# Optimization experiments

Hardware: AMD Instinct MI355X
Metric: run time of the kernel (lower is better)

Reference implementation:

```python
import jax, jax.numpy as jnp
import numpy as np

B, K, IN_DIM, H, D = 8, 4096, 512, 8, 64  # batch, tokens, in_dim, heads, per-head dim


def setup_inputs() -> dict:
    key = jax.random.key(0)
    ks = jax.random.split(key, 8)
    s = 0.02
    return {
        "x": jax.random.normal(ks[0], (B, K, IN_DIM), jnp.float32),
        "y": jax.random.normal(ks[1], (B, K, IN_DIM), jnp.float32),
        "Wq": jax.random.normal(ks[2], (IN_DIM, H * D), jnp.float32) * s,
        "bq": jnp.zeros((H * D,), jnp.float32),
        "Wk": jax.random.normal(ks[3], (IN_DIM, H * D), jnp.float32) * s,
        "bk": jnp.zeros((H * D,), jnp.float32),
        "Wv": jax.random.normal(ks[4], (IN_DIM, H * D), jnp.float32) * s,
        "bv": jnp.zeros((H * D,), jnp.float32),
        "Wp": jax.random.normal(ks[5], (IN_DIM, D), jnp.float32) * s,
        "gamma": jax.random.uniform(ks[6], (H, 1, 1, 1), jnp.float32) + 0.001,
    }


def _heads(t):
    # (B, K, H*D) -> (H, B, K, D); matches split_cat(t, D, dim=2, cat dim=0) head-major layout
    b, k, _ = t.shape
    return t.reshape(b, k, H, D).transpose(2, 0, 1, 3)


def reference(x, y, Wq, bq, Wk, bk, Wv, bv, Wp, gamma):
    q = _heads(x @ Wq + bq)   # (H,B,K,D)
    kk = _heads(x @ Wk + bk)  # (H,B,K,D)
    v = _heads(y @ Wv + bv)   # (H,B,K,D)
    # energy = q^T k contracted over tokens -> (H,B,D,D)
    energy = jnp.einsum('hbkd,hbke->hbde', q, kk)
    attn = jax.nn.softmax(energy, axis=-1)
    # out = v @ attn^T : out[k,q] = sum_e v[k,e] * attn[q,e]
    out = jnp.einsum('hbke,hbqe->hbkq', v, attn)  # (H,B,K,D)
    yp = y @ Wp  # projection(y): (B,K,D)
    out = (gamma * out + yp[None]) / (1.0 + gamma)
    return out.transpose(1, 0, 2, 3)  # (B,H,K,D)
```

## Files before the change

kernel.cpp:

```cpp
#include <hip/hip_runtime.h>

#define B_ 8
#define K_ 4096
#define IN_ 512
#define H_ 8
#define D_ 64
#define HD_ 512

typedef short bf16x8 __attribute__((ext_vector_type(8)));
typedef float f32x4 __attribute__((ext_vector_type(4)));
typedef unsigned short u16;
typedef unsigned short us8v __attribute__((ext_vector_type(8)));
typedef unsigned short us4v __attribute__((ext_vector_type(4)));

__device__ inline u16 f2bf_rn(float f) {
  unsigned u = __float_as_uint(f);
  u += 0x7fffu + ((u >> 16) & 1u);
  return (u16)(u >> 16);
}
__device__ inline float bf2f(u16 h) {
  return __uint_as_float(((unsigned)h) << 16);
}


__global__ __launch_bounds__(256) void k_cvt_x(const float* __restrict__ x,
                                               u16* __restrict__ xt_hi,
                                               u16* __restrict__ xt_lo,
                                               float* __restrict__ svec) {
  const int kt = blockIdx.x, ct = blockIdx.y, b = blockIdx.z;
  __shared__ float Xs[64][65];
  const int tid = threadIdx.x;
  const float* src = x + ((size_t)b * K_ + kt * 64) * IN_ + ct * 64;
#pragma unroll
  for (int r = 0; r < 4; ++r) {
    int idx = tid + 256 * r;
    int k = idx >> 4, c4 = (idx & 15) * 4;
    f32x4 v = *(const f32x4*)(src + (size_t)k * IN_ + c4);
    Xs[k][c4 + 0] = v[0];
    Xs[k][c4 + 1] = v[1];
    Xs[k][c4 + 2] = v[2];
    Xs[k][c4 + 3] = v[3];
  }
  __syncthreads();
  if (tid < 64) {
    float s = 0.f;
#pragma unroll
    for (int k = 0; k < 64; ++k) s += Xs[k][tid];
    atomicAdd(&svec[b * IN_ + ct * 64 + tid], s);
  }
#pragma unroll
  for (int r = 0; r < 2; ++r) {
    int idx = tid + 256 * r;
    int c = idx >> 3, ck = (idx & 7) * 8;
    us8v hv, lv;
#pragma unroll
    for (int j = 0; j < 8; ++j) {
      float f = Xs[ck + j][c];
      u16 h = f2bf_rn(f);
      float lo = f - bf2f(h);
      hv[j] = h;
      lv[j] = f2bf_rn(lo);
    }
    size_t off = ((size_t)(b * IN_ + ct * 64 + c)) * K_ + kt * 64 + ck;
    *(us8v*)(xt_hi + off) = hv;
    *(us8v*)(xt_lo + off) = lv;
  }
}

__global__ __launch_bounds__(256) void k_cvt_y(const float* __restrict__ y,
                                               u16* __restrict__ yb) {
  size_t i = ((size_t)blockIdx.x * 256 + threadIdx.x) * 8;
  f32x4 v0 = *(const f32x4*)(y + i);
  f32x4 v1 = *(const f32x4*)(y + i + 4);
  us8v o;
  o[0] = f2bf_rn(v0[0]); o[1] = f2bf_rn(v0[1]);
  o[2] = f2bf_rn(v0[2]); o[3] = f2bf_rn(v0[3]);
  o[4] = f2bf_rn(v1[0]); o[5] = f2bf_rn(v1[1]);
  o[6] = f2bf_rn(v1[2]); o[7] = f2bf_rn(v1[3]);
  *(us8v*)(yb + i) = o;
}

__global__ __launch_bounds__(256) void k_cvt_w(
    const float* __restrict__ Wq, const float* __restrict__ Wk,
    u16* __restrict__ Wqt_hi, u16* __restrict__ Wqt_lo,
    u16* __restrict__ Wkt_hi, u16* __restrict__ Wkt_lo) {
  const int ti = blockIdx.x, tj = blockIdx.y;
  const float* src = blockIdx.z ? Wk : Wq;
  u16* dhi = blockIdx.z ? Wkt_hi : Wqt_hi;
  u16* dlo = blockIdx.z ? Wkt_lo : Wqt_lo;
  __shared__ float T[64][65];
  const int tid = threadIdx.x;
#pragma unroll
  for (int r = 0; r < 4; ++r) {
    int idx = tid + 256 * r;
    int rr = idx >> 4, c4 = (idx & 15) * 4;
    f32x4 v = *(const f32x4*)(src + (size_t)(tj * 64 + rr) * 512 + ti * 64 + c4);
    T[rr][c4 + 0] = v[0]; T[rr][c4 + 1] = v[1];
    T[rr][c4 + 2] = v[2]; T[rr][c4 + 3] = v[3];
  }
  __syncthreads();
#pragma unroll
  for (int r = 0; r < 2; ++r) {
    int idx = tid + 256 * r;
    int d = idx >> 3, ck = (idx & 7) * 8;
    us8v hv, lv;
#pragma unroll
    for (int j = 0; j < 8; ++j) {
      float f = T[ck + j][d];
      u16 h = f2bf_rn(f);
      hv[j] = h;
      lv[j] = f2bf_rn(f - bf2f(h));
    }
    size_t off = (size_t)(ti * 64 + d) * 512 + tj * 64 + ck;
    *(us8v*)(dhi + off) = hv;
    *(us8v*)(dlo + off) = lv;
  }
}

#define GP 72

__global__ __launch_bounds__(256, 2) void k_gram_mfma(
    const u16* __restrict__ xt_hi, const u16* __restrict__ xt_lo,
    float* __restrict__ G) {
  int pp = blockIdx.x, ti = 0;
  while (pp >= 4 - ti) { pp -= 4 - ti; ++ti; }
  const int tj = ti + pp;
  const int b = blockIdx.y >> 3, kc = blockIdx.y & 7;
  __shared__ u16 Pih[128 * GP], Pil[128 * GP], Pjh[128 * GP], Pjl[128 * GP];
  const int tid = threadIdx.x;
  const int wave = tid >> 6, lane = tid & 63;
  const int wm = wave & 1, wn = wave >> 1;
  const int m16 = lane & 15, quad = lane >> 4;
  const size_t base_i = ((size_t)(b * IN_ + ti * 128)) * K_;
  const size_t base_j = ((size_t)(b * IN_ + tj * 128)) * K_;
  f32x4 zf = {0.f, 0.f, 0.f, 0.f};
  f32x4 acc[4][4];
#pragma unroll
  for (int mt = 0; mt < 4; ++mt)
#pragma unroll
    for (int nt = 0; nt < 4; ++nt) acc[mt][nt] = zf;
  const int kbeg = kc * 512, kend = kbeg + 512;

  us8v sih[4], sil[4], sjh[4], sjl[4];
  auto GLOAD = [&](int k0) {
#pragma unroll
    for (int r = 0; r < 4; ++r) {
      int idx = tid + 256 * r;
      int row = idx >> 3, ck = (idx & 7) * 8;
      size_t gi = base_i + (size_t)row * K_ + k0 + ck;
      size_t gj = base_j + (size_t)row * K_ + k0 + ck;
      sih[r] = *(const us8v*)(xt_hi + gi);
      sil[r] = *(const us8v*)(xt_lo + gi);
      sjh[r] = *(const us8v*)(xt_hi + gj);
      sjl[r] = *(const us8v*)(xt_lo + gj);
    }
  };
  auto SWRITE = [&]() {
#pragma unroll
    for (int r = 0; r < 4; ++r) {
      int idx = tid + 256 * r;
      int row = idx >> 3, ck = (idx & 7) * 8;
      int lo = row * GP + ck;
      *(us8v*)&Pih[lo] = sih[r];
      *(us8v*)&Pil[lo] = sil[r];
      *(us8v*)&Pjh[lo] = sjh[r];
      *(us8v*)&Pjl[lo] = sjl[r];
    }
  };

  GLOAD(kbeg);
  SWRITE();
  __syncthreads();
  for (int k0 = kbeg; k0 < kend; k0 += 64) {
    const bool more = (k0 + 64 < kend);
    if (more) GLOAD(k0 + 64);
#pragma unroll
    for (int kk = 0; kk < 64; kk += 32) {
      bf16x8 ah[4], al[4], bh[4], bl[4];
#pragma unroll
      for (int t = 0; t < 4; ++t) {
        int ar = (wm * 64 + t * 16 + m16) * GP + kk + quad * 8;
        ah[t] = *(const bf16x8*)&Pih[ar];
        al[t] = *(const bf16x8*)&Pil[ar];
        int br = (wn * 64 + t * 16 + m16) * GP + kk + quad * 8;
        bh[t] = *(const bf16x8*)&Pjh[br];
        bl[t] = *(const bf16x8*)&Pjl[br];
      }
#pragma unroll
      for (int mt = 0; mt < 4; ++mt)
#pragma unroll
        for (int nt = 0; nt < 4; ++nt) {
          acc[mt][nt] = __builtin_amdgcn_mfma_f32_16x16x32_bf16(
              ah[mt], bh[nt], acc[mt][nt], 0, 0, 0);
          acc[mt][nt] = __builtin_amdgcn_mfma_f32_16x16x32_bf16(
              ah[mt], bl[nt], acc[mt][nt], 0, 0, 0);
          acc[mt][nt] = __builtin_amdgcn_mfma_f32_16x16x32_bf16(
              al[mt], bh[nt], acc[mt][nt], 0, 0, 0);
        }
    }
    if (more) {
      __syncthreads();
      SWRITE();
      __syncthreads();
    }
  }
  float* Gb = G + (size_t)b * IN_ * IN_;
#pragma unroll
  for (int mt = 0; mt < 4; ++mt)
#pragma unroll
    for (int nt = 0; nt < 4; ++nt)
#pragma unroll
      for (int r = 0; r < 4; ++r) {
        int gi = ti * 128 + wm * 64 + mt * 16 + quad * 4 + r;
        int gj = tj * 128 + wn * 64 + nt * 16 + m16;
        atomicAdd(&Gb[(size_t)gi * IN_ + gj], acc[mt][nt][r]);
      }
}

__global__ __launch_bounds__(256) void k_cvt_g(const float* __restrict__ G,
                                               u16* __restrict__ Ghi,
                                               u16* __restrict__ Glo) {
  const int ti = blockIdx.x, tj = blockIdx.y, b = blockIdx.z;
  if (tj < ti) return;
  const float* Gb = G + (size_t)b * IN_ * IN_;
  u16* ghb = Ghi + (size_t)b * IN_ * IN_;
  u16* glb = Glo + (size_t)b * IN_ * IN_;
  __shared__ float T[64][65];
  const int tid = threadIdx.x;
#pragma unroll
  for (int r = 0; r < 4; ++r) {
    int idx = tid + 256 * r;
    int rr = idx >> 4, c4 = (idx & 15) * 4;
    f32x4 v = *(const f32x4*)(Gb + (size_t)(ti * 64 + rr) * IN_ + tj * 64 + c4);
    T[rr][c4 + 0] = v[0]; T[rr][c4 + 1] = v[1];
    T[rr][c4 + 2] = v[2]; T[rr][c4 + 3] = v[3];
  }
  __syncthreads();
#pragma unroll
  for (int r = 0; r < 2; ++r) {
    int idx = tid + 256 * r;
    int rr = idx >> 3, ck = (idx & 7) * 8;
    us8v hv, lv;
#pragma unroll
    for (int j = 0; j < 8; ++j) {
      float f = T[rr][ck + j];
      u16 h = f2bf_rn(f);
      hv[j] = h;
      lv[j] = f2bf_rn(f - bf2f(h));
    }
    size_t off = (size_t)(ti * 64 + rr) * IN_ + tj * 64 + ck;
    *(us8v*)(ghb + off) = hv;
    *(us8v*)(glb + off) = lv;
  }
  if (ti != tj) {
#pragma unroll
    for (int r = 0; r < 2; ++r) {
      int idx = tid + 256 * r;
      int rr = idx >> 3, ck = (idx & 7) * 8;
      us8v hv, lv;
#pragma unroll
      for (int j = 0; j < 8; ++j) {
        float f = T[ck + j][rr];
        u16 h = f2bf_rn(f);
        hv[j] = h;
        lv[j] = f2bf_rn(f - bf2f(h));
      }
      size_t off = (size_t)(tj * 64 + rr) * IN_ + ti * 64 + ck;
      *(us8v*)(ghb + off) = hv;
      *(us8v*)(glb + off) = lv;
    }
  }
}

__global__ __launch_bounds__(256) void k_aall_mfma(
    const u16* __restrict__ Wqt_hi, const u16* __restrict__ Wqt_lo,
    const u16* __restrict__ Ghi, const u16* __restrict__ Glo,
    u16* __restrict__ Ahi, u16* __restrict__ Alo) {
  const int ct = blockIdx.x;
  const int hb = blockIdx.y;
  const int h = hb >> 3, b = hb & 7;
  __shared__ u16 S[4 * 64 * GP];
  u16* Ah = S;
  u16* Al = S + 64 * GP;
  u16* Bh = S + 2 * 64 * GP;
  u16* Bl = S + 3 * 64 * GP;
  const int tid = threadIdx.x;
  const int wave = tid >> 6, lane = tid & 63;
  const int m16 = lane & 15, quad = lane >> 4;
  const u16* Abase_h = Wqt_hi + (size_t)(h * 64) * IN_;
  const u16* Abase_l = Wqt_lo + (size_t)(h * 64) * IN_;
  const u16* Bbase_h = Ghi + (size_t)b * IN_ * IN_ + (size_t)(ct * 64) * IN_;
  const u16* Bbase_l = Glo + (size_t)b * IN_ * IN_ + (size_t)(ct * 64) * IN_;
  f32x4 zf = {0.f, 0.f, 0.f, 0.f};
  f32x4 acc[4] = {zf, zf, zf, zf};
  for (int k0 = 0; k0 < IN_; k0 += 64) {
    __syncthreads();
#pragma unroll
    for (int r = 0; r < 2; ++r) {
      int idx = tid + 256 * r;
      int row = idx >> 3, ck = (idx & 7) * 8;
      int lo = row * GP + ck;
      *(us8v*)&Ah[lo] = *(const us8v*)(Abase_h + (size_t)row * IN_ + k0 + ck);
      *(us8v*)&Al[lo] = *(const us8v*)(Abase_l + (size_t)row * IN_ + k0 + ck);
      *(us8v*)&Bh[lo] = *(const us8v*)(Bbase_h + (size_t)row * IN_ + k0 + ck);
      *(us8v*)&Bl[lo] = *(const us8v*)(Bbase_l + (size_t)row * IN_ + k0 + ck);
    }
    __syncthreads();
#pragma unroll
    for (int kk = 0; kk < 64; kk += 32) {
      int arow = (wave * 16 + m16) * GP + kk + quad * 8;
      bf16x8 ah = *(const bf16x8*)&Ah[arow];
      bf16x8 al = *(const bf16x8*)&Al[arow];
#pragma unroll
      for (int n = 0; n < 4; ++n) {
        int brow = (n * 16 + m16) * GP + kk + quad * 8;
        bf16x8 bh = *(const bf16x8*)&Bh[brow];
        bf16x8 bl = *(const bf16x8*)&Bl[brow];
        acc[n] = __builtin_amdgcn_mfma_f32_16x16x32_bf16(ah, bh, acc[n], 0, 0, 0);
        acc[n] = __builtin_amdgcn_mfma_f32_16x16x32_bf16(ah, bl, acc[n], 0, 0, 0);
        acc[n] = __builtin_amdgcn_mfma_f32_16x16x32_bf16(al, bh, acc[n], 0, 0, 0);
      }
    }
  }
  __syncthreads();
  float* Sf = (float*)S;
#pragma unroll
  for (int n = 0; n < 4; ++n)
#pragma unroll
    for (int r = 0; r < 4; ++r) {
      int d = wave * 16 + quad * 4 + r;
      int cc = n * 16 + m16;
      Sf[d * 68 + cc] = acc[n][r];
    }
  __syncthreads();
#pragma unroll
  for (int r = 0; r < 2; ++r) {
    int idx = tid + 256 * r;
    int d = idx >> 3, ck = (idx & 7) * 8;
    us8v hv, lv;
#pragma unroll
    for (int j = 0; j < 8; ++j) {
      float f = Sf[d * 68 + ck + j];
      u16 h2 = f2bf_rn(f);
      hv[j] = h2;
      lv[j] = f2bf_rn(f - bf2f(h2));
    }
    size_t off = ((size_t)hb * 64 + d) * IN_ + ct * 64 + ck;
    *(us8v*)(Ahi + off) = hv;
    *(us8v*)(Alo + off) = lv;
  }
}

__global__ __launch_bounds__(256) void k_attn3(
    const u16* __restrict__ Ahi, const u16* __restrict__ Alo,
    const u16* __restrict__ Wqt_hi, const u16* __restrict__ Wqt_lo,
    const u16* __restrict__ Wkt_hi, const u16* __restrict__ Wkt_lo,
    const float* __restrict__ Wv, const float* __restrict__ Wp,
    const float* __restrict__ bq, const float* __restrict__ bk,
    const float* __restrict__ bv, const float* __restrict__ gamma,
    const float* __restrict__ svec, u16* __restrict__ Wft,
    float* __restrict__ bfin) {
  const int h = blockIdx.x, b = blockIdx.y;
  const int hb = h * B_ + b;
  const int tid = threadIdx.x;
  const int wave = tid >> 6, lane = tid & 63;
  const int m16 = lane & 15, quad = lane >> 4;
  __shared__ u16 S[4 * 64 * GP];
  __shared__ float Esh[64][65];
  __shared__ float t1[64], t2[64];
  u16* Ah = S;
  u16* Al = S + 64 * GP;
  u16* Bh = S + 2 * 64 * GP;
  u16* Bl = S + 3 * 64 * GP;

  if (tid < 64) {
    float s = 0.f;
    const u16* wh = Wkt_hi + (size_t)(h * 64 + tid) * IN_;
    const u16* wl = Wkt_lo + (size_t)(h * 64 + tid) * IN_;
    for (int c = 0; c < IN_; ++c)
      s += svec[b * IN_ + c] * (bf2f(wh[c]) + bf2f(wl[c]));
    t1[tid] = s;
  } else if (tid < 128) {
    int d = tid - 64;
    float s = 0.f;
    const u16* wh = Wqt_hi + (size_t)(h * 64 + d) * IN_;
    const u16* wl = Wqt_lo + (size_t)(h * 64 + d) * IN_;
    for (int c = 0; c < IN_; ++c)
      s += svec[b * IN_ + c] * (bf2f(wh[c]) + bf2f(wl[c]));
    t2[d] = s;
  }

  const u16* Abase_h = Ahi + (size_t)hb * 64 * IN_;
  const u16* Abase_l = Alo + (size_t)hb * 64 * IN_;
  const u16* Bbase_h = Wkt_hi + (size_t)(h * 64) * IN_;
  const u16* Bbase_l = Wkt_lo + (size_t)(h * 64) * IN_;
  f32x4 zf = {0.f, 0.f, 0.f, 0.f};
  f32x4 acc[4] = {zf, zf, zf, zf};
  for (int k0 = 0; k0 < IN_; k0 += 64) {
    __syncthreads();
#pragma unroll
    for (int r = 0; r < 2; ++r) {
      int idx = tid + 256 * r;
      int row = idx >> 3, ck = (idx & 7) * 8;
      int lo = row * GP + ck;
      *(us8v*)&Ah[lo] = *(const us8v*)(Abase_h + (size_t)row * IN_ + k0 + ck);
      *(us8v*)&Al[lo] = *(const us8v*)(Abase_l + (size_t)row * IN_ + k0 + ck);
      *(us8v*)&Bh[lo] = *(const us8v*)(Bbase_h + (size_t)row * IN_ + k0 + ck);
      *(us8v*)&Bl[lo] = *(const us8v*)(Bbase_l + (size_t)row * IN_ + k0 + ck);
    }
    __syncthreads();
#pragma unroll
    for (int kk = 0; kk < 64; kk += 32) {
      int arow = (wave * 16 + m16) * GP + kk + quad * 8;
      bf16x8 ah = *(const bf16x8*)&Ah[arow];
      bf16x8 al = *(const bf16x8*)&Al[arow];
#pragma unroll
      for (int n = 0; n < 4; ++n) {
        int brow = (n * 16 + m16) * GP + kk + quad * 8;
        bf16x8 bh = *(const bf16x8*)&Bh[brow];
        bf16x8 bl = *(const bf16x8*)&Bl[brow];
        acc[n] = __builtin_amdgcn_mfma_f32_16x16x32_bf16(ah, bh, acc[n], 0, 0, 0);
        acc[n] = __builtin_amdgcn_mfma_f32_16x16x32_bf16(ah, bl, acc[n], 0, 0, 0);
        acc[n] = __builtin_amdgcn_mfma_f32_16x16x32_bf16(al, bh, acc[n], 0, 0, 0);
      }
    }
  }
  __syncthreads();
#pragma unroll
  for (int n = 0; n < 4; ++n)
#pragma unroll
    for (int r = 0; r < 4; ++r) {
      int d = wave * 16 + quad * 4 + r;
      int e = n * 16 + m16;
      float bqd = bq[h * D_ + d], bke = bk[h * D_ + e];
      Esh[d][e] = acc[n][r] + bqd * t1[e] + t2[d] * bke + (float)K_ * bqd * bke;
    }
  __syncthreads();
  const float g = gamma[h];
  const float inv1g = 1.f / (1.f + g);
  if (tid < 64) {
    float m = -1e30f;
    for (int e = 0; e < 64; ++e) m = fmaxf(m, Esh[tid][e]);
    float ssum = 0.f;
    for (int e = 0; e < 64; ++e) {
      float p = __expf(Esh[tid][e] - m);
      Esh[tid][e] = p;
      ssum += p;
    }
    float inv = 1.f / ssum;
    float bsum = 0.f;
    for (int e = 0; e < 64; ++e) {
      Esh[tid][e] *= inv;
      bsum += bv[h * D_ + e] * Esh[tid][e];
    }
    bfin[hb * D_ + tid] = g * bsum * inv1g;
  }
  __syncthreads();

  bf16x8 bfr[4][2];
#pragma unroll
  for (int n = 0; n < 4; ++n)
#pragma unroll
    for (int kk = 0; kk < 2; ++kk)
#pragma unroll
      for (int j = 0; j < 8; ++j)
        bfr[n][kk][j] = f2bf_rn(Esh[n * 16 + m16][kk * 32 + quad * 8 + j]);

  u16* Wf = Wft + (size_t)hb * D_ * IN_;
#pragma unroll
  for (int mt = 0; mt < 8; ++mt) {
    f32x4 a4[4] = {zf, zf, zf, zf};
#pragma unroll
    for (int kk = 0; kk < 2; ++kk) {
      int c = wave * 128 + mt * 16 + m16;
      const float* wv = Wv + (size_t)c * HD_ + h * D_ + kk * 32 + quad * 8;
      f32x4 v0 = *(const f32x4*)wv;
      f32x4 v1 = *(const f32x4*)(wv + 4);
      bf16x8 af;
      af[0] = f2bf_rn(v0[0]); af[1] = f2bf_rn(v0[1]);
      af[2] = f2bf_rn(v0[2]); af[3] = f2bf_rn(v0[3]);
      af[4] = f2bf_rn(v1[0]); af[5] = f2bf_rn(v1[1]);
      af[6] = f2bf_rn(v1[2]); af[7] = f2bf_rn(v1[3]);
#pragma unroll
      for (int n = 0; n < 4; ++n)
        a4[n] = __builtin_amdgcn_mfma_f32_16x16x32_bf16(af, bfr[n][kk], a4[n], 0, 0, 0);
    }
    int cb = wave * 128 + mt * 16 + quad * 4;
#pragma unroll
    for (int n = 0; n < 4; ++n) {
      int q = n * 16 + m16;
      us4v st;
#pragma unroll
      for (int r = 0; r < 4; ++r) {
        float val = (g * a4[n][r] + Wp[(size_t)(cb + r) * D_ + q]) * inv1g;
        st[r] = f2bf_rn(val);
      }
      *(us4v*)(Wf + (size_t)q * IN_ + cb) = st;
    }
  }
}

__global__ __launch_bounds__(256, 2) void k_out_mfma(
    const u16* __restrict__ yb, const u16* __restrict__ Wft,
    const float* __restrict__ bfin, float* __restrict__ out) {
  const int kt = blockIdx.x;
  const int b = blockIdx.y & 7, hq = blockIdx.y >> 3;
  const int h0 = hq * 2;
  __shared__ u16 Wsh[2][2 * 64 * 64];
  const int tid = threadIdx.x, wave = tid >> 6, lane = tid & 63;
  const int m16 = lane & 15, quad = lane >> 4;
  const int swz = (m16 & 7) << 3;

  us8v stg[4];
  auto LOAD = [&](int c0) {
#pragma unroll
    for (int r = 0; r < 4; ++r) {
      int idx = tid + 256 * r;
      int row = idx >> 3, ck = (idx & 7) * 8;
      int i = row >> 6, q = row & 63;
      const u16* src =
          Wft + ((size_t)((h0 + i) * 8 + b) * 64 + q) * IN_ + c0 + ck;
      stg[r] = *(const us8v*)src;
    }
  };
  auto WRITE = [&](int buf) {
#pragma unroll
    for (int r = 0; r < 4; ++r) {
      int idx = tid + 256 * r;
      int row = idx >> 3, ck = (idx & 7) * 8;
      *(us8v*)&Wsh[buf][row * 64 + (ck ^ ((row & 7) << 3))] = stg[r];
    }
  };
  bf16x8 yf[2][4];
  auto LOADY = [&](bf16x8 (*yd)[4], int c0) {
#pragma unroll
    for (int kk = 0; kk < 2; ++kk)
#pragma unroll
      for (int ms = 0; ms < 4; ++ms) {
        int row = kt * 256 + wave * 64 + ms * 16 + m16;
        yd[kk][ms] = *(const bf16x8*)(yb + ((size_t)b * K_ + row) * IN_ + c0 +
                                      kk * 32 + quad * 8);
      }
  };

  f32x4 zf = {0.f, 0.f, 0.f, 0.f};
  f32x4 acc[4][2][4];
#pragma unroll
  for (int ms = 0; ms < 4; ++ms)
#pragma unroll
    for (int i = 0; i < 2; ++i)
#pragma unroll
      for (int nt = 0; nt < 4; ++nt) acc[ms][i][nt] = zf;

  LOAD(0);
  LOADY(yf, 0);
  WRITE(0);
  __syncthreads();
  int cur = 0;
  for (int c0 = 0; c0 < IN_; c0 += 64) {
    const bool more = (c0 + 64 < IN_);
    bf16x8 yn[2][4];
    if (more) {
      LOAD(c0 + 64);
      LOADY(yn, c0 + 64);
    }
#pragma unroll
    for (int kk = 0; kk < 2; ++kk)
#pragma unroll
      for (int i = 0; i < 2; ++i)
#pragma unroll
        for (int nt = 0; nt < 4; ++nt) {
          int brow = i * 64 + nt * 16 + m16;
          bf16x8 bb = *(const bf16x8*)&Wsh[cur][brow * 64 +
                                               ((kk * 32 + quad * 8) ^ swz)];
#pragma unroll
          for (int ms = 0; ms < 4; ++ms)
            acc[ms][i][nt] = __builtin_amdgcn_mfma_f32_16x16x32_bf16(
                yf[kk][ms], bb, acc[ms][i][nt], 0, 0, 0);
        }
    if (more) {
      WRITE(cur ^ 1);
      __syncthreads();
      cur ^= 1;
#pragma unroll
      for (int kk = 0; kk < 2; ++kk)
#pragma unroll
        for (int ms = 0; ms < 4; ++ms) yf[kk][ms] = yn[kk][ms];
    }
  }

#pragma unroll
  for (int i = 0; i < 2; ++i) {
    float* ob = out + (((size_t)b * H_ + h0 + i) * K_) * D_;
    const int hb = (h0 + i) * 8 + b;
#pragma unroll
    for (int ms = 0; ms < 4; ++ms)
#pragma unroll
      for (int nt = 0; nt < 4; ++nt) {
        int col = nt * 16 + m16;
        float bf = bfin[hb * D_ + col];
#pragma unroll
        for (int r = 0; r < 4; ++r) {
          int row = kt * 256 + wave * 64 + ms * 16 + quad * 4 + r;
          ob[(size_t)row * D_ + col] = acc[ms][i][nt][r] + bf;
        }
      }
  }
}

__global__ __launch_bounds__(256) void k_gram(const float* __restrict__ x,
                                              float* __restrict__ G,
                                              float* __restrict__ svec) {
  const int it = blockIdx.x, jt = blockIdx.y, b = blockIdx.z;
  if (jt < it) return;
  __shared__ float Xi[16][64];
  __shared__ float Xj[16][64];
  const float* Xb = x + (size_t)b * K_ * IN_;
  const int tx = threadIdx.x, ty = threadIdx.y;
  const int tid = ty * 16 + tx;
  const int i0 = it * 64, j0 = jt * 64;
  const bool diag = (it == jt);
  float acc[4][4] = {};
  float ssum = 0.f;
  for (int k0 = 0; k0 < K_; k0 += 16) {
#pragma unroll
    for (int r = 0; r < 4; ++r) {
      int idx = tid + 256 * r;
      int kk = idx >> 6, cc = idx & 63;
      const float* row = Xb + (size_t)(k0 + kk) * IN_;
      Xi[kk][cc] = row[i0 + cc];
      Xj[kk][cc] = row[j0 + cc];
    }
    __syncthreads();
#pragma unroll
    for (int kk = 0; kk < 16; ++kk) {
      float a[4], bb[4];
#pragma unroll
      for (int u = 0; u < 4; ++u) a[u] = Xi[kk][ty * 4 + u];
#pragma unroll
      for (int u = 0; u < 4; ++u) bb[u] = Xj[kk][tx * 4 + u];
#pragma unroll
      for (int u = 0; u < 4; ++u)
#pragma unroll
        for (int w = 0; w < 4; ++w) acc[u][w] += a[u] * bb[w];
    }
    if (diag && tid < 64) {
#pragma unroll
      for (int kk = 0; kk < 16; ++kk) ssum += Xi[kk][tid];
    }
    __syncthreads();
  }
  float* Gb = G + (size_t)b * IN_ * IN_;
#pragma unroll
  for (int u = 0; u < 4; ++u)
#pragma unroll
    for (int w = 0; w < 4; ++w) {
      int gi = i0 + ty * 4 + u, gj = j0 + tx * 4 + w;
      Gb[(size_t)gi * IN_ + gj] = acc[u][w];
      if (!diag) Gb[(size_t)gj * IN_ + gi] = acc[u][w];
    }
  if (diag && tid < 64) svec[b * IN_ + i0 + tid] = ssum;
}

__global__ __launch_bounds__(256) void k_aall(const float* __restrict__ Wq,
                                              const float* __restrict__ G,
                                              float* __restrict__ Aall) {
  const int jt = blockIdx.x;
  const int h = blockIdx.y, b = blockIdx.z;
  __shared__ float Ws[16][64];
  __shared__ float Gs[16][64];
  const float* Gb = G + (size_t)b * IN_ * IN_;
  const int tx = threadIdx.x, ty = threadIdx.y;
  const int tid = ty * 16 + tx;
  float acc[4][4] = {};
  for (int c0 = 0; c0 < IN_; c0 += 16) {
#pragma unroll
    for (int r = 0; r < 4; ++r) {
      int idx = tid + 256 * r;
      int kk = idx >> 6, cc = idx & 63;
      Ws[kk][cc] = Wq[(size_t)(c0 + kk) * HD_ + h * D_ + cc];
      Gs[kk][cc] = Gb[(size_t)(c0 + kk) * IN_ + jt * 64 + cc];
    }
    __syncthreads();
#pragma unroll
    for (int kk = 0; kk < 16; ++kk) {
      float a[4], bb[4];
#pragma unroll
      for (int u = 0; u < 4; ++u) a[u] = Ws[kk][ty * 4 + u];
#pragma unroll
      for (int u = 0; u < 4; ++u) bb[u] = Gs[kk][tx * 4 + u];
#pragma unroll
      for (int u = 0; u < 4; ++u)
#pragma unroll
        for (int w = 0; w < 4; ++w) acc[u][w] += a[u] * bb[w];
    }
    __syncthreads();
  }
  const int hb = h * B_ + b;
  float* Ahb = Aall + (size_t)hb * D_ * IN_;
#pragma unroll
  for (int u = 0; u < 4; ++u)
#pragma unroll
    for (int w = 0; w < 4; ++w)
      Ahb[(size_t)(ty * 4 + u) * IN_ + jt * 64 + tx * 4 + w] = acc[u][w];
}

__global__ __launch_bounds__(256) void k_attn_f32(
    const float* __restrict__ Wq, const float* __restrict__ Wk,
    const float* __restrict__ Wv, const float* __restrict__ Wp,
    const float* __restrict__ bq, const float* __restrict__ bk,
    const float* __restrict__ bv, const float* __restrict__ gamma,
    const float* __restrict__ Aall, const float* __restrict__ svec,
    float* __restrict__ Wfin, float* __restrict__ bfin) {
  const int h = blockIdx.x, b = blockIdx.y;
  const int hb = h * B_ + b;
  const int tx = threadIdx.x, ty = threadIdx.y;
  const int tid = ty * 16 + tx;
  __shared__ float Ast[64][17];
  __shared__ float Ws[16][64];
  __shared__ float Esh[64][65];
  __shared__ float t1[64], t2[64];
  const float* Ahb = Aall + (size_t)hb * D_ * IN_;
  if (tid < 64) {
    float a2 = 0.f;
    for (int c = 0; c < IN_; ++c)
      a2 += svec[b * IN_ + c] * Wk[(size_t)c * HD_ + h * D_ + tid];
    t1[tid] = a2;
  } else if (tid < 128) {
    int d = tid - 64;
    float a2 = 0.f;
    for (int c = 0; c < IN_; ++c)
      a2 += svec[b * IN_ + c] * Wq[(size_t)c * HD_ + h * D_ + d];
    t2[d] = a2;
  }
  float acc[4][4] = {};
  for (int c0 = 0; c0 < IN_; c0 += 16) {
#pragma unroll
    for (int r = 0; r < 4; ++r) {
      int idx = tid + 256 * r;
      int dd = idx >> 4, kk = idx & 15;
      Ast[dd][kk] = Ahb[(size_t)dd * IN_ + c0 + kk];
      int kk2 = idx >> 6, ee = idx & 63;
      Ws[kk2][ee] = Wk[(size_t)(c0 + kk2) * HD_ + h * D_ + ee];
    }
    __syncthreads();
#pragma unroll
    for (int kk = 0; kk < 16; ++kk) {
      float a[4], bb[4];
#pragma unroll
      for (int u = 0; u < 4; ++u) a[u] = Ast[ty * 4 + u][kk];
#pragma unroll
      for (int u = 0; u < 4; ++u) bb[u] = Ws[kk][tx * 4 + u];
#pragma unroll
      for (int u = 0; u < 4; ++u)
#pragma unroll
        for (int w = 0; w < 4; ++w) acc[u][w] += a[u] * bb[w];
    }
    __syncthreads();
  }
#pragma unroll
  for (int u = 0; u < 4; ++u) {
    int d = ty * 4 + u;
    float bqd = bq[h * D_ + d];
    float t2d = t2[d];
#pragma unroll
    for (int w = 0; w < 4; ++w) {
      int e = tx * 4 + w;
      float bke = bk[h * D_ + e];
      Esh[d][e] = acc[u][w] + bqd * t1[e] + t2d * bke + (float)K_ * bqd * bke;
    }
  }
  __syncthreads();
  if (tid < 64) {
    float m = -1e30f;
    for (int e = 0; e < 64; ++e) m = fmaxf(m, Esh[tid][e]);
    float ssum = 0.f;
    for (int e = 0; e < 64; ++e) {
      float p = __expf(Esh[tid][e] - m);
      Esh[tid][e] = p;
      ssum += p;
    }
    float inv = 1.f / ssum;
    for (int e = 0; e < 64; ++e) Esh[tid][e] *= inv;
  }
  __syncthreads();
  const float g = gamma[h];
  const float inv1g = 1.f / (1.f + g);
  if (tid < 64) {
    float a2 = 0.f;
    for (int e = 0; e < 64; ++e) a2 += bv[h * D_ + e] * Esh[tid][e];
    bfin[hb * D_ + tid] = g * a2 * inv1g;
  }
  float* Wf = Wfin + (size_t)hb * IN_ * D_;
  for (int it2 = 0; it2 < 128; ++it2) {
    int idx = tid + 256 * it2;
    int c = idx >> 6, q = idx & 63;
    const float* Wvr = Wv + (size_t)c * HD_ + h * D_;
    float a2 = 0.f;
#pragma unroll
    for (int e = 0; e < 64; ++e) a2 += Wvr[e] * Esh[q][e];
    Wf[idx] = (g * a2 + Wp[(size_t)c * D_ + q]) * inv1g;
  }
}

__global__ __launch_bounds__(256) void k_out_f32(const float* __restrict__ y,
                                                 const float* __restrict__ Wfin,
                                                 const float* __restrict__ bfin,
                                                 float* __restrict__ out) {
  const int kt = blockIdx.x;
  const int hb = blockIdx.y;
  const int h = hb >> 3, b = hb & 7;
  __shared__ float Ys[64][17];
  __shared__ float Ws[16][64];
  const int tx = threadIdx.x, ty = threadIdx.y;
  const int tid = ty * 16 + tx;
  const float* Yb = y + (size_t)b * K_ * IN_;
  const float* Wf = Wfin + (size_t)hb * IN_ * D_;
  const int k0 = kt * 64;
  float acc[4][4] = {};
  for (int c0 = 0; c0 < IN_; c0 += 16) {
#pragma unroll
    for (int r = 0; r < 4; ++r) {
      int idx = tid + 256 * r;
      int rr = idx >> 4, kk = idx & 15;
      Ys[rr][kk] = Yb[(size_t)(k0 + rr) * IN_ + c0 + kk];
      int kk2 = idx >> 6, qq = idx & 63;
      Ws[kk2][qq] = Wf[(size_t)(c0 + kk2) * D_ + qq];
    }
    __syncthreads();
#pragma unroll
    for (int kk = 0; kk < 16; ++kk) {
      float a[4], bb[4];
#pragma unroll
      for (int u = 0; u < 4; ++u) a[u] = Ys[ty * 4 + u][kk];
#pragma unroll
      for (int u = 0; u < 4; ++u) bb[u] = Ws[kk][tx * 4 + u];
#pragma unroll
      for (int u = 0; u < 4; ++u)
#pragma unroll
        for (int w = 0; w < 4; ++w) acc[u][w] += a[u] * bb[w];
    }
    __syncthreads();
  }
  float* ob = out + (((size_t)b * H_ + h) * K_ + k0) * D_;
#pragma unroll
  for (int u = 0; u < 4; ++u) {
    int k = ty * 4 + u;
#pragma unroll
    for (int w = 0; w < 4; ++w) {
      int q = tx * 4 + w;
      ob[(size_t)k * D_ + q] = acc[u][w] + bfin[hb * D_ + q];
    }
  }
}

extern "C" void kernel_launch(void* const* d_in, const int* in_sizes, int n_in,
                              void* d_out, int out_size, void* d_ws,
                              size_t ws_size, hipStream_t stream) {
  const float* x = (const float*)d_in[0];
  const float* y = (const float*)d_in[1];
  const float* Wq = (const float*)d_in[2];
  const float* bq = (const float*)d_in[3];
  const float* Wk = (const float*)d_in[4];
  const float* bk = (const float*)d_in[5];
  const float* Wv = (const float*)d_in[6];
  const float* bv = (const float*)d_in[7];
  const float* Wp = (const float*)d_in[8];
  const float* gm = (const float*)d_in[9];
  float* out = (float*)d_out;

  const size_t NEED = 86016000;
  if (ws_size >= NEED) {
    char* w = (char*)d_ws;
    u16* xt_hi = (u16*)(w);
    u16* Ahi = (u16*)(w);
    u16* Alo = (u16*)(w + 4194304);
    u16* Wft = (u16*)(w + 8388608);
    u16* xt_lo = (u16*)(w + 33554432);
    u16* yb = (u16*)(w + 33554432);
    float* G = (float*)(w + 67108864);
    u16* Ghi = (u16*)(w + 75497472);
    u16* Glo = (u16*)(w + 79691776);
    u16* Wqt_hi = (u16*)(w + 83886080);
    u16* Wqt_lo = (u16*)(w + 84410368);
    u16* Wkt_hi = (u16*)(w + 84934656);
    u16* Wkt_lo = (u16*)(w + 85458944);
    float* bfin = (float*)(w + 85983232);
    float* svec = (float*)(w + 85999616);

    hipMemsetAsync(G, 0, 8388608, stream);
    hipMemsetAsync(svec, 0, 16384, stream);
    k_cvt_w<<<dim3(8, 8, 2), 256, 0, stream>>>(Wq, Wk, Wqt_hi, Wqt_lo, Wkt_hi,
                                               Wkt_lo);
    k_cvt_x<<<dim3(64, 8, 8), 256, 0, stream>>>(x, xt_hi, xt_lo, svec);
    k_gram_mfma<<<dim3(10, 64), 256, 0, stream>>>(xt_hi, xt_lo, G);
    k_cvt_y<<<dim3(8192), 256, 0, stream>>>(y, yb);
    k_cvt_g<<<dim3(8, 8, 8), 256, 0, stream>>>(G, Ghi, Glo);
    k_aall_mfma<<<dim3(8, 64), 256, 0, stream>>>(Wqt_hi, Wqt_lo, Ghi, Glo, Ahi,
                                                 Alo);
    k_attn3<<<dim3(8, 8), 256, 0, stream>>>(Ahi, Alo, Wqt_hi, Wqt_lo, Wkt_hi,
                                            Wkt_lo, Wv, Wp, bq, bk, bv, gm,
                                            svec, Wft, bfin);
    k_out_mfma<<<dim3(16, 32), 256, 0, stream>>>(yb, Wft, bfin, out);
  } else {
    float* ws = (float*)d_ws;
    float* G = ws;
    float* Aall = ws + 2097152;
    float* Wfin = ws + 4194304;
    float* bfin = ws + 6291456;
    float* svec = ws + 6295552;
    dim3 blk(16, 16);
    k_gram<<<dim3(8, 8, 8), blk, 0, stream>>>(x, G, svec);
    k_aall<<<dim3(8, 8, 8), blk, 0, stream>>>(Wq, G, Aall);
    k_attn_f32<<<dim3(8, 8), blk, 0, stream>>>(Wq, Wk, Wv, Wp, bq, bk, bv, gm,
                                               Aall, svec, Wfin, bfin);
    k_out_f32<<<dim3(64, 64), blk, 0, stream>>>(y, Wfin, bfin, out);
  }
}
```

Baseline: 343.3 us.

## Use direct global-to-LDS loads with XOR swizzle in gram and Aall kernels

Replaces register-staged global loads plus LDS stores in the gram and Aall MFMA kernels with global_load_lds direct copies, using an XOR-swizzled unpadded LDS layout to avoid bank conflicts. On diagonal gram tiles it skips loading the j-panel and reads the i-panel for both operands. It flattens the gram grid so the k-chunks of a tile are adjacent, and vectorizes the svec dot products in k_attn3. In exchange the gram kernel loses its software prefetch double-buffering, so loads are no longer overlapped with MFMA work.

Measured after the change: 332.4 us. 1.03x faster.

```diff
diff --git a/kernel.cpp b/kernel.cpp
--- a/kernel.cpp
+++ b/kernel.cpp
@@ -20,6 +20,12 @@
 }
 __device__ inline float bf2f(u16 h) {
   return __uint_as_float(((unsigned)h) << 16);
+}
+
+__device__ inline void gl_lds16(const u16* g, u16* l) {
+  __builtin_amdgcn_global_load_lds(
+      (const __attribute__((address_space(1))) unsigned int*)g,
+      (__attribute__((address_space(3))) unsigned int*)l, 16, 0, 0);
 }
 
 
@@ -122,17 +128,31 @@
 __global__ __launch_bounds__(256, 2) void k_gram_mfma(
     const u16* __restrict__ xt_hi, const u16* __restrict__ xt_lo,
     float* __restrict__ G) {
-  int pp = blockIdx.x, ti = 0;
+  const int fid = blockIdx.x;
+  const int kc = fid & 7;
+  const int slot = fid >> 3;
+  const int b = slot / 10;
+  int pp = slot - b * 10, ti = 0;
   while (pp >= 4 - ti) { pp -= 4 - ti; ++ti; }
   const int tj = ti + pp;
-  const int b = blockIdx.y >> 3, kc = blockIdx.y & 7;
-  __shared__ u16 Pih[128 * GP], Pil[128 * GP], Pjh[128 * GP], Pjl[128 * GP];
+  const bool diag = (ti == tj);
+  __shared__ u16 P[4 * 128 * 64];
+  u16* Pih = P;
+  u16* Pil = P + 128 * 64;
+  u16* Pjh = P + 2 * 128 * 64;
+  u16* Pjl = P + 3 * 128 * 64;
   const int tid = threadIdx.x;
   const int wave = tid >> 6, lane = tid & 63;
   const int wm = wave & 1, wn = wave >> 1;
   const int m16 = lane & 15, quad = lane >> 4;
   const size_t base_i = ((size_t)(b * IN_ + ti * 128)) * K_;
   const size_t base_j = ((size_t)(b * IN_ + tj * 128)) * K_;
+  const int lrow = lane >> 3;
+  const int lcol = ((lane & 7) * 8) ^ (lrow << 3);
+  const size_t loff = (size_t)lrow * K_ + lcol;
+  const u16* PBh = diag ? Pih : Pjh;
+  const u16* PBl = diag ? Pil : Pjl;
+
   f32x4 zf = {0.f, 0.f, 0.f, 0.f};
   f32x4 acc[4][4];
 #pragma unroll
@@ -141,50 +161,33 @@
     for (int nt = 0; nt < 4; ++nt) acc[mt][nt] = zf;
   const int kbeg = kc * 512, kend = kbeg + 512;
 
-  us8v sih[4], sil[4], sjh[4], sjl[4];
-  auto GLOAD = [&](int k0) {
+  for (int k0 = kbeg; k0 < kend; k0 += 64) {
+    __syncthreads();
 #pragma unroll
     for (int r = 0; r < 4; ++r) {
-      int idx = tid + 256 * r;
-      int row = idx >> 3, ck = (idx & 7) * 8;
-      size_t gi = base_i + (size_t)row * K_ + k0 + ck;
-      size_t gj = base_j + (size_t)row * K_ + k0 + ck;
-      sih[r] = *(const us8v*)(xt_hi + gi);
-      sil[r] = *(const us8v*)(xt_lo + gi);
-      sjh[r] = *(const us8v*)(xt_hi + gj);
-      sjl[r] = *(const us8v*)(xt_lo + gj);
-    }
-  };
-  auto SWRITE = [&]() {
-#pragma unroll
-    for (int r = 0; r < 4; ++r) {
-      int idx = tid + 256 * r;
-      int row = idx >> 3, ck = (idx & 7) * 8;
-      int lo = row * GP + ck;
-      *(us8v*)&Pih[lo] = sih[r];
-      *(us8v*)&Pil[lo] = sil[r];
-      *(us8v*)&Pjh[lo] = sjh[r];
-      *(us8v*)&Pjl[lo] = sjl[r];
-    }
-  };
-
-  GLOAD(kbeg);
-  SWRITE();
-  __syncthreads();
-  for (int k0 = kbeg; k0 < kend; k0 += 64) {
-    const bool more = (k0 + 64 < kend);
-    if (more) GLOAD(k0 + 64);
+      int rg = wave * 4 + r;
+      size_t go = (size_t)(rg * 8) * K_ + k0 + loff;
+      int lo = rg * 8 * 64;
+      gl_lds16(xt_hi + base_i + go, &Pih[lo]);
+      gl_lds16(xt_lo + base_i + go, &Pil[lo]);
+      if (!diag) {
+        gl_lds16(xt_hi + base_j + go, &Pjh[lo]);
+        gl_lds16(xt_lo + base_j + go, &Pjl[lo]);
+      }
+    }
+    __syncthreads();
 #pragma unroll
     for (int kk = 0; kk < 64; kk += 32) {
+      const int ac = (kk + quad * 8) ^ ((m16 & 7) << 3);
       bf16x8 ah[4], al[4], bh[4], bl[4];
 #pragma unroll
       for (int t = 0; t < 4; ++t) {
-        int ar = (wm * 64 + t * 16 + m16) * GP + kk + quad * 8;
+        int ar = (wm * 64 + t * 16 + m16) * 64 + ac;
         ah[t] = *(const bf16x8*)&Pih[ar];
         al[t] = *(const bf16x8*)&Pil[ar];
-        int br = (wn * 64 + t * 16 + m16) * GP + kk + quad * 8;
-        bh[t] = *(const bf16x8*)&Pjh[br];
-        bl[t] = *(const bf16x8*)&Pjl[br];
+        int br = (wn * 64 + t * 16 + m16) * 64 + ac;
+        bh[t] = *(const bf16x8*)&PBh[br];
+        bl[t] = *(const bf16x8*)&PBl[br];
       }
 #pragma unroll
       for (int mt = 0; mt < 4; ++mt)
@@ -197,11 +200,6 @@
           acc[mt][nt] = __builtin_amdgcn_mfma_f32_16x16x32_bf16(
               al[mt], bh[nt], acc[mt][nt], 0, 0, 0);
         }
-    }
-    if (more) {
-      __syncthreads();
-      SWRITE();
-      __syncthreads();
     }
   }
   float* Gb = G + (size_t)b * IN_ * IN_;
@@ -279,11 +277,11 @@
   const int ct = blockIdx.x;
   const int hb = blockIdx.y;
   const int h = hb >> 3, b = hb & 7;
-  __shared__ u16 S[4 * 64 * GP];
+  __shared__ u16 S[4 * 64 * 64];
   u16* Ah = S;
-  u16* Al = S + 64 * GP;
-  u16* Bh = S + 2 * 64 * GP;
-  u16* Bl = S + 3 * 64 * GP;
+  u16* Al = S + 64 * 64;
+  u16* Bh = S + 2 * 64 * 64;
+  u16* Bl = S + 3 * 64 * 64;
   const int tid = threadIdx.x;
   const int wave = tid >> 6, lane = tid & 63;
   const int m16 = lane & 15, quad = lane >> 4;
@@ -291,29 +289,33 @@
   const u16* Abase_l = Wqt_lo + (size_t)(h * 64) * IN_;
   const u16* Bbase_h = Ghi + (size_t)b * IN_ * IN_ + (size_t)(ct * 64) * IN_;
   const u16* Bbase_l = Glo + (size_t)b * IN_ * IN_ + (size_t)(ct * 64) * IN_;
+  const int lrow = lane >> 3;
+  const int lcol = ((lane & 7) * 8) ^ (lrow << 3);
+  const size_t loff = (size_t)lrow * IN_ + lcol;
   f32x4 zf = {0.f, 0.f, 0.f, 0.f};
   f32x4 acc[4] = {zf, zf, zf, zf};
   for (int k0 = 0; k0 < IN_; k0 += 64) {
     __syncthreads();
 #pragma unroll
     for (int r = 0; r < 2; ++r) {
-      int idx = tid + 256 * r;
-      int row = idx >> 3, ck = (idx & 7) * 8;
-      int lo = row * GP + ck;
-      *(us8v*)&Ah[lo] = *(const us8v*)(Abase_h + (size_t)row * IN_ + k0 + ck);
-      *(us8v*)&Al[lo] = *(const us8v*)(Abase_l + (size_t)row * IN_ + k0 + ck);
-      *(us8v*)&Bh[lo] = *(const us8v*)(Bbase_h + (size_t)row * IN_ + k0 + ck);
-      *(us8v*)&Bl[lo] = *(const us8v*)(Bbase_l + (size_t)row * IN_ + k0 + ck);
+      int rg = wave * 2 + r;
+      size_t go = (size_t)(rg * 8) * IN_ + k0 + loff;
+      int lo = rg * 8 * 64;
+      gl_lds16(Abase_h + go, &Ah[lo]);
+      gl_lds16(Abase_l + go, &Al[lo]);
+      gl_lds16(Bbase_h + go, &Bh[lo]);
+      gl_lds16(Bbase_l + go, &Bl[lo]);
     }
     __syncthreads();
 #pragma unroll
     for (int kk = 0; kk < 64; kk += 32) {
-      int arow = (wave * 16 + m16) * GP + kk + quad * 8;
+      const int ac = (kk + quad * 8) ^ ((m16 & 7) << 3);
+      int arow = (wave * 16 + m16) * 64 + ac;
       bf16x8 ah = *(const bf16x8*)&Ah[arow];
       bf16x8 al = *(const bf16x8*)&Al[arow];
 #pragma unroll
       for (int n = 0; n < 4; ++n) {
-        int brow = (n * 16 + m16) * GP + kk + quad * 8;
+        int brow = (n * 16 + m16) * 64 + ac;
         bf16x8 bh = *(const bf16x8*)&Bh[brow];
         bf16x8 bl = *(const bf16x8*)&Bl[brow];
         acc[n] = __builtin_amdgcn_mfma_f32_16x16x32_bf16(ah, bh, acc[n], 0, 0, 0);
@@ -377,16 +379,28 @@
     float s = 0.f;
     const u16* wh = Wkt_hi + (size_t)(h * 64 + tid) * IN_;
     const u16* wl = Wkt_lo + (size_t)(h * 64 + tid) * IN_;
-    for (int c = 0; c < IN_; ++c)
-      s += svec[b * IN_ + c] * (bf2f(wh[c]) + bf2f(wl[c]));
+    const float* sv = svec + b * IN_;
+    for (int c = 0; c < IN_; c += 8) {
+      us8v hv = *(const us8v*)(wh + c);
+      us8v lv = *(const us8v*)(wl + c);
+#pragma unroll
+      for (int j = 0; j < 8; ++j)
+        s += sv[c + j] * (bf2f(hv[j]) + bf2f(lv[j]));
+    }
     t1[tid] = s;
   } else if (tid < 128) {
     int d = tid - 64;
     float s = 0.f;
     const u16* wh = Wqt_hi + (size_t)(h * 64 + d) * IN_;
     const u16* wl = Wqt_lo + (size_t)(h * 64 + d) * IN_;
-    for (int c = 0; c < IN_; ++c)
-      s += svec[b * IN_ + c] * (bf2f(wh[c]) + bf2f(wl[c]));
+    const float* sv = svec + b * IN_;
+    for (int c = 0; c < IN_; c += 8) {
+      us8v hv = *(const us8v*)(wh + c);
+      us8v lv = *(const us8v*)(wl + c);
+#pragma unroll
+      for (int j = 0; j < 8; ++j)
+        s += sv[c + j] * (bf2f(hv[j]) + bf2f(lv[j]));
+    }
     t2[d] = s;
   }
 
@@ -893,7 +907,7 @@
     k_cvt_w<<<dim3(8, 8, 2), 256, 0, stream>>>(Wq, Wk, Wqt_hi, Wqt_lo, Wkt_hi,
                                                Wkt_lo);
     k_cvt_x<<<dim3(64, 8, 8), 256, 0, stream>>>(x, xt_hi, xt_lo, svec);
-    k_gram_mfma<<<dim3(10, 64), 256, 0, stream>>>(xt_hi, xt_lo, G);
+    k_gram_mfma<<<dim3(640), 256, 0, stream>>>(xt_hi, xt_lo, G);
     k_cvt_y<<<dim3(8192), 256, 0, stream>>>(y, yb);
     k_cvt_g<<<dim3(8, 8, 8), 256, 0, stream>>>(G, Ghi, Glo);
     k_aall_mfma<<<dim3(8, 64), 256, 0, stream>>>(Wqt_hi, Wqt_lo, Ghi, Glo, Ahi,
```
